# Kernel tuning notes

Hardware: AMD Instinct MI355X
Metric: run time of the kernel (lower is better)

The kernel has to match this reference:

```python
import jax, jax.numpy as jnp
import numpy as np

INPUT_SIZE = 512   # num_embeddings == RNN input feature dim
SEQ = INPUT_SIZE // 4   # 128, embedding dim == RNN seq_len
HID = 12
OUT = 3
B = 2048


def setup_inputs() -> dict:
    key = jax.random.key(0)
    ks = jax.random.split(key, 12)
    s = 0.1
    x = jax.random.randint(ks[0], (B, INPUT_SIZE), 0, INPUT_SIZE)
    emb = jax.random.normal(ks[1], (INPUT_SIZE, SEQ), dtype=jnp.float32) * s
    w_ih_f = jax.random.normal(ks[2], (HID, INPUT_SIZE), dtype=jnp.float32) * s
    w_hh_f = jax.random.normal(ks[3], (HID, HID), dtype=jnp.float32) * s
    b_ih_f = jax.random.normal(ks[4], (HID,), dtype=jnp.float32) * s
    b_hh_f = jax.random.normal(ks[5], (HID,), dtype=jnp.float32) * s
    w_ih_r = jax.random.normal(ks[6], (HID, INPUT_SIZE), dtype=jnp.float32) * s
    w_hh_r = jax.random.normal(ks[7], (HID, HID), dtype=jnp.float32) * s
    b_ih_r = jax.random.normal(ks[8], (HID,), dtype=jnp.float32) * s
    b_hh_r = jax.random.normal(ks[9], (HID,), dtype=jnp.float32) * s
    fc_w = jax.random.normal(ks[10], (OUT, 2 * HID), dtype=jnp.float32) * s
    fc_b = jax.random.normal(ks[11], (OUT,), dtype=jnp.float32) * s
    return {"x": x, "emb": emb,
            "w_ih_f": w_ih_f, "w_hh_f": w_hh_f, "b_ih_f": b_ih_f, "b_hh_f": b_hh_f,
            "w_ih_r": w_ih_r, "w_hh_r": w_hh_r, "b_ih_r": b_ih_r, "b_hh_r": b_hh_r,
            "fc_w": fc_w, "fc_b": fc_b}


def reference(x, emb, w_ih_f, w_hh_f, b_ih_f, b_hh_f,
              w_ih_r, w_hh_r, b_ih_r, b_hh_r, fc_w, fc_b):
    # embedding lookup: (B, INPUT_SIZE) -> (B, INPUT_SIZE, SEQ)
    e = emb[x]
    # view(-1, input_size, seq) is a no-op on this contiguous shape; swapaxes(1,2)
    xs = jnp.swapaxes(e, 1, 2)  # (B, SEQ, INPUT_SIZE): seq_len=SEQ, feat=INPUT_SIZE

    # forward-direction tanh RNN: precompute input projections, scan the recurrence
    pre = jnp.einsum('bsi,hi->sbh', xs, w_ih_f) + b_ih_f  # (SEQ, B, HID)

    def step(h, p):
        h = jnp.tanh(p + h @ w_hh_f.T + b_hh_f)
        return h, None

    h0 = jnp.zeros((xs.shape[0], HID), dtype=xs.dtype)
    h_fwd, _ = jax.lax.scan(step, h0, pre)  # final forward hidden (B, HID)

    # reverse-direction output at the LAST timestep = one step from zero hidden
    # on x_{T-1} (only out[:, -1, :] is consumed by the module)
    h_bwd = jnp.tanh(xs[:, -1, :] @ w_ih_r.T + b_ih_r + b_hh_r)  # (B, HID)

    out_last = jnp.concatenate([h_fwd, h_bwd], axis=-1)  # (B, 2*HID)
    return out_last @ fc_w.T + fc_b  # (B, OUT)
```

## Files before the change

kernel.cpp:

```cpp
#include <hip/hip_runtime.h>
#include <hip/hip_bf16.h>

#define B_N     2048
#define IN_N    512
#define SEQ_N   128
#define HID_N   12
#define HP_N    16
#define OUT_N   3

typedef __attribute__((ext_vector_type(8))) short short8;
typedef __attribute__((ext_vector_type(4))) float f32x4;
typedef unsigned int uint;
typedef unsigned short ushort;

__device__ __forceinline__ float fast_tanh(float x) {
    float e = __builtin_amdgcn_exp2f(x * 2.8853900817779268f);
    return 1.0f - 2.0f * __builtin_amdgcn_rcpf(e + 1.0f);
}

__device__ __forceinline__ ushort f2bf(float f) {
    uint u = __float_as_uint(f);
    u += 0x7fffu + ((u >> 16) & 1u);
    return (ushort)(u >> 16);
}

__device__ __forceinline__ float bf2f(ushort s) {
    return __uint_as_float(((uint)s) << 16);
}

__global__ __launch_bounds__(256) void k_prep(
    const float* __restrict__ emb, const float* __restrict__ w_ih_f,
    const float* __restrict__ w_ih_r,
    ushort* __restrict__ embB, ushort* __restrict__ wBT, ushort* __restrict__ wRT)
{
    int tid = blockIdx.x * 256 + threadIdx.x;
    float4 e = ((const float4*)emb)[tid];
    uint2 o;
    o.x = (uint)f2bf(e.x) | ((uint)f2bf(e.y) << 16);
    o.y = (uint)f2bf(e.z) | ((uint)f2bf(e.w) << 16);
    ((uint2*)embB)[tid] = o;
    if (tid < 16 * IN_N) {
        bool live = tid < HID_N * IN_N;
        wBT[tid] = live ? f2bf(w_ih_f[tid]) : (ushort)0;
        wRT[tid] = live ? f2bf(w_ih_r[tid]) : (ushort)0;
    }
}

__global__ __launch_bounds__(256, 2) void k_pre(
    const int* __restrict__ x, const ushort* __restrict__ embB,
    const ushort* __restrict__ wBT, const ushort* __restrict__ wRT,
    const float* __restrict__ b_ih_r, const float* __restrict__ b_hh_r,
    ushort* __restrict__ preB, float* __restrict__ rev)
{
    __shared__ int xb[IN_N];
    __shared__ __align__(16) ushort As[128 * 128];

    const int t = threadIdx.x;
    const int b = blockIdx.x;

    ((int2*)xb)[t] = ((const int2*)(x + b * IN_N))[t];
    __syncthreads();

    const int l      = t & 63;
    const int w      = t >> 6;
    const int lane16 = l & 15;
    const int quad   = l >> 4;
    const int il     = w * 32 + quad * 8;
    const int wg     = w * 4 + quad;
    const int wsx    = lane16 & 7;

    f32x4 acc[2] = {{0.f,0.f,0.f,0.f},{0.f,0.f,0.f,0.f}};
    f32x4 accR   = {0.f,0.f,0.f,0.f};

    uint R[8][4];

    #pragma unroll
    for (int j = 0; j < 8; ++j) {
        const uint4 v = *(const uint4*)(embB + (size_t)xb[il + j] * SEQ_N + lane16 * 8);
        R[j][0] = v.x; R[j][1] = v.y; R[j][2] = v.z; R[j][3] = v.w;
    }

    for (int c = 0; c < 4; ++c) {
        short8 bfr[4], bfrR[4];
        #pragma unroll
        for (int ks = 0; ks < 4; ++ks) {
            bfr[ks]  = *(const short8*)(wBT + lane16 * IN_N + c * 128 + ks * 32 + quad * 8);
            bfrR[ks] = *(const short8*)(wRT + lane16 * IN_N + c * 128 + ks * 32 + quad * 8);
        }

        if (c) __syncthreads();

        #pragma unroll
        for (int p = 0; p < 8; ++p) {
            const uint sel = (p & 1) ? 0x07060302u : 0x05040100u;
            const int pv = p >> 1;
            uint u0 = __builtin_amdgcn_perm(R[1][pv], R[0][pv], sel);
            uint u1 = __builtin_amdgcn_perm(R[3][pv], R[2][pv], sel);
            uint u2 = __builtin_amdgcn_perm(R[5][pv], R[4][pv], sel);
            uint u3 = __builtin_amdgcn_perm(R[7][pv], R[6][pv], sel);
            const int s = lane16 * 8 + p;
            *(uint4*)&As[(size_t)s * 128 + (size_t)(wg ^ wsx) * 8] =
                make_uint4(u0, u1, u2, u3);
        }

        if (c < 3) {
            const int ibase = (c + 1) * 128 + il;
            #pragma unroll
            for (int j = 0; j < 8; ++j) {
                const uint4 v = *(const uint4*)(embB + (size_t)xb[ibase + j] * SEQ_N + lane16 * 8);
                R[j][0] = v.x; R[j][1] = v.y; R[j][2] = v.z; R[j][3] = v.w;
            }
        }
        __syncthreads();

        #pragma unroll
        for (int tt = 0; tt < 2; ++tt) {
            const int row = (w * 2 + tt) * 16 + lane16;
            const int rsx = (row >> 3) & 7;
            #pragma unroll
            for (int ks = 0; ks < 4; ++ks) {
                short8 af = *(const short8*)&As[(size_t)row * 128 +
                                                (size_t)(((ks * 4 + quad) ^ rsx)) * 8];
                acc[tt] = __builtin_amdgcn_mfma_f32_16x16x32_bf16(af, bfr[ks], acc[tt], 0, 0, 0);
                if (tt == 1)
                    accR = __builtin_amdgcn_mfma_f32_16x16x32_bf16(af, bfrR[ks], accR, 0, 0, 0);
            }
        }
    }

    if (lane16 < HID_N) {
        #pragma unroll
        for (int tt = 0; tt < 2; ++tt) {
            #pragma unroll
            for (int r = 0; r < 4; ++r) {
                int s = (w * 2 + tt) * 16 + quad * 4 + r;
                preB[((size_t)b * SEQ_N + s) * HP_N + lane16] = f2bf(acc[tt][r]);
            }
        }
        if (w == 3 && quad == 3)
            rev[b * HP_N + lane16] =
                fast_tanh(accR[3] + b_ih_r[lane16] + b_hh_r[lane16]);
    }
}

__global__ __launch_bounds__(256) void k_rnn(
    const ushort* __restrict__ preB, const float* __restrict__ rev,
    const float* __restrict__ w_hh_f,
    const float* __restrict__ b_ih_f, const float* __restrict__ b_hh_f,
    const float* __restrict__ fc_w, const float* __restrict__ fc_b,
    float* __restrict__ out)
{
    __shared__ float ho[16][40];

    const int tid = threadIdx.x;
    const int l   = tid & 63;
    const int j   = l & 15;
    const int jj  = (j < 12) ? j : 0;
    const int gid = tid >> 4;
    const int b   = blockIdx.x * 16 + gid;
    const int baseaddr = (l & 48) << 2;

    const float4* wr = (const float4*)(w_hh_f + jj * 12);
    float4 w0 = wr[0], w1 = wr[1], w2 = wr[2];
    float W[12] = {w0.x, w0.y, w0.z, w0.w, w1.x, w1.y, w1.z, w1.w,
                   w2.x, w2.y, w2.z, w2.w};
    const float bias = b_ih_f[jj] + b_hh_f[jj];

    const ushort* pb = preB + (size_t)b * SEQ_N * HP_N + j;
    ushort pq[8];
    #pragma unroll
    for (int k = 0; k < 8; ++k) pq[k] = pb[k * HP_N];

    float h = 0.f;
    for (int s8 = 0; s8 < 16; ++s8) {
        #pragma unroll
        for (int k = 0; k < 8; ++k) {
            int s = s8 * 8 + k;
            float p = bf2f(pq[k]) + bias;
            pq[k] = pb[((s + 8) & 127) * HP_N];
            int hb = __float_as_int(h);
            float hk[12];
            #pragma unroll
            for (int kk = 0; kk < 12; ++kk)
                hk[kk] = __int_as_float(__builtin_amdgcn_ds_bpermute(baseaddr + 4 * kk, hb));
            float c0 = p, c1 = 0.f, c2 = 0.f;
            #pragma unroll
            for (int u = 0; u < 4; ++u) {
                c0 = __builtin_fmaf(W[u],     hk[u],     c0);
                c1 = __builtin_fmaf(W[4 + u], hk[4 + u], c1);
                c2 = __builtin_fmaf(W[8 + u], hk[8 + u], c2);
            }
            h = fast_tanh(c0 + c1 + c2);
        }
    }

    ho[gid][j]      = h;
    ho[gid][20 + j] = rev[b * HP_N + j];
    if (j < OUT_N) {
        const float* fw = fc_w + j * 24;
        float o = fc_b[j];
        #pragma unroll
        for (int k = 0; k < 12; ++k)
            o += fw[k] * ho[gid][k] + fw[12 + k] * ho[gid][20 + k];
        out[b * OUT_N + j] = o;
    }
}

extern "C" void kernel_launch(void* const* d_in, const int* in_sizes, int n_in,
                              void* d_out, int out_size, void* d_ws, size_t ws_size,
                              hipStream_t stream) {
    const int*   x      = (const int*)  d_in[0];
    const float* emb    = (const float*)d_in[1];
    const float* w_ih_f = (const float*)d_in[2];
    const float* w_hh_f = (const float*)d_in[3];
    const float* b_ih_f = (const float*)d_in[4];
    const float* b_hh_f = (const float*)d_in[5];
    const float* w_ih_r = (const float*)d_in[6];
    const float* b_ih_r = (const float*)d_in[8];
    const float* b_hh_r = (const float*)d_in[9];
    const float* fc_w   = (const float*)d_in[10];
    const float* fc_b   = (const float*)d_in[11];
    float* out = (float*)d_out;

    ushort* preB = (ushort*)d_ws;
    float*  rev  = (float*)((char*)d_ws + 8388608);
    ushort* embB = (ushort*)((char*)d_ws + 8519680);
    ushort* wBT  = (ushort*)((char*)d_ws + 8650752);
    ushort* wRT  = (ushort*)((char*)d_ws + 8667136);

    k_prep<<<64,   256, 0, stream>>>(emb, w_ih_f, w_ih_r, embB, wBT, wRT);
    k_pre <<<B_N,  256, 0, stream>>>(x, embB, wBT, wRT, b_ih_r, b_hh_r, preB, rev);
    k_rnn <<<B_N/16,256,0, stream>>>(preB, rev, w_hh_f, b_ih_f, b_hh_f, fc_w, fc_b, out);
}
```

Measured before the change: 138.2 us.

## Prepack MFMA weight fragments, fix LDS swizzle conflicts, raise k_pre occupancy

The ih weights are now prepacked into per-lane MFMA B-fragment order, so each lane reads one contiguous 16-byte chunk per k-step instead of strided rows. The LDS swizzle for the A tile now also XORs in the row's low bits, to spread the ds_write/ds_read traffic across banks. launch_bounds for k_pre goes from 2 to 4 blocks per SM to allow more occupancy, at the risk of register pressure or spills with the R[8][4] staging array.

```diff
diff --git a/kernel.cpp b/kernel.cpp
--- a/kernel.cpp
+++ b/kernel.cpp
@@ -31,7 +31,7 @@
 __global__ __launch_bounds__(256) void k_prep(
     const float* __restrict__ emb, const float* __restrict__ w_ih_f,
     const float* __restrict__ w_ih_r,
-    ushort* __restrict__ embB, ushort* __restrict__ wBT, ushort* __restrict__ wRT)
+    ushort* __restrict__ embB, ushort* __restrict__ wP)
 {
     int tid = blockIdx.x * 256 + threadIdx.x;
     float4 e = ((const float4*)emb)[tid];
@@ -39,16 +39,21 @@
     o.x = (uint)f2bf(e.x) | ((uint)f2bf(e.y) << 16);
     o.y = (uint)f2bf(e.z) | ((uint)f2bf(e.w) << 16);
     ((uint2*)embB)[tid] = o;
-    if (tid < 16 * IN_N) {
-        bool live = tid < HID_N * IN_N;
-        wBT[tid] = live ? f2bf(w_ih_f[tid]) : (ushort)0;
-        wRT[tid] = live ? f2bf(w_ih_r[tid]) : (ushort)0;
-    }
-}
-
-__global__ __launch_bounds__(256, 2) void k_pre(
+
+    int j   = tid & 7;
+    int l   = (tid >> 3) & 63;
+    int src = (tid >> 9) & 1;
+    int cks = tid >> 10;
+    int h   = l & 15;
+    int i   = (cks >> 2) * 128 + (cks & 3) * 32 + (l >> 4) * 8 + j;
+    const float* wsrc = src ? w_ih_r : w_ih_f;
+    wP[(((size_t)cks * 2 + src) * 64 + l) * 8 + j] =
+        (h < HID_N) ? f2bf(wsrc[h * IN_N + i]) : (ushort)0;
+}
+
+__global__ __launch_bounds__(256, 4) void k_pre(
     const int* __restrict__ x, const ushort* __restrict__ embB,
-    const ushort* __restrict__ wBT, const ushort* __restrict__ wRT,
+    const ushort* __restrict__ wP,
     const float* __restrict__ b_ih_r, const float* __restrict__ b_hh_r,
     ushort* __restrict__ preB, float* __restrict__ rev)
 {
@@ -67,7 +72,7 @@
     const int quad   = l >> 4;
     const int il     = w * 32 + quad * 8;
     const int wg     = w * 4 + quad;
-    const int wsx    = lane16 & 7;
+    const int l7     = lane16 & 7;
 
     f32x4 acc[2] = {{0.f,0.f,0.f,0.f},{0.f,0.f,0.f,0.f}};
     f32x4 accR   = {0.f,0.f,0.f,0.f};
@@ -84,8 +89,9 @@
         short8 bfr[4], bfrR[4];
         #pragma unroll
         for (int ks = 0; ks < 4; ++ks) {
-            bfr[ks]  = *(const short8*)(wBT + lane16 * IN_N + c * 128 + ks * 32 + quad * 8);
-            bfrR[ks] = *(const short8*)(wRT + lane16 * IN_N + c * 128 + ks * 32 + quad * 8);
+            const ushort* wp = wP + ((size_t)(c * 4 + ks) * 128 + l) * 8;
+            bfr[ks]  = *(const short8*)(wp);
+            bfrR[ks] = *(const short8*)(wp + 512);
         }
 
         if (c) __syncthreads();
@@ -98,8 +104,9 @@
             uint u1 = __builtin_amdgcn_perm(R[3][pv], R[2][pv], sel);
             uint u2 = __builtin_amdgcn_perm(R[5][pv], R[4][pv], sel);
             uint u3 = __builtin_amdgcn_perm(R[7][pv], R[6][pv], sel);
-            const int s = lane16 * 8 + p;
-            *(uint4*)&As[(size_t)s * 128 + (size_t)(wg ^ wsx) * 8] =
+            const int s    = lane16 * 8 + p;
+            const int slot = wg ^ p ^ l7;
+            *(uint4*)&As[(size_t)s * 128 + (size_t)slot * 8] =
                 make_uint4(u0, u1, u2, u3);
         }
 
@@ -116,11 +123,11 @@
         #pragma unroll
         for (int tt = 0; tt < 2; ++tt) {
             const int row = (w * 2 + tt) * 16 + lane16;
-            const int rsx = (row >> 3) & 7;
+            const int fr  = (row & 7) ^ ((row >> 3) & 7);
             #pragma unroll
             for (int ks = 0; ks < 4; ++ks) {
-                short8 af = *(const short8*)&As[(size_t)row * 128 +
-                                                (size_t)(((ks * 4 + quad) ^ rsx)) * 8];
+                const int slot = (ks * 4 + quad) ^ fr;
+                short8 af = *(const short8*)&As[(size_t)row * 128 + (size_t)slot * 8];
                 acc[tt] = __builtin_amdgcn_mfma_f32_16x16x32_bf16(af, bfr[ks], acc[tt], 0, 0, 0);
                 if (tt == 1)
                     accR = __builtin_amdgcn_mfma_f32_16x16x32_bf16(af, bfrR[ks], accR, 0, 0, 0);
@@ -225,10 +232,9 @@
     ushort* preB = (ushort*)d_ws;
     float*  rev  = (float*)((char*)d_ws + 8388608);
     ushort* embB = (ushort*)((char*)d_ws + 8519680);
-    ushort* wBT  = (ushort*)((char*)d_ws + 8650752);
-    ushort* wRT  = (ushort*)((char*)d_ws + 8667136);
-
-    k_prep<<<64,   256, 0, stream>>>(emb, w_ih_f, w_ih_r, embB, wBT, wRT);
-    k_pre <<<B_N,  256, 0, stream>>>(x, embB, wBT, wRT, b_ih_r, b_hh_r, preB, rev);
+    ushort* wP   = (ushort*)((char*)d_ws + 8650752);
+
+    k_prep<<<64,   256, 0, stream>>>(emb, w_ih_f, w_ih_r, embB, wP);
+    k_pre <<<B_N,  256, 0, stream>>>(x, embB, wP, b_ih_r, b_hh_r, preB, rev);
     k_rnn <<<B_N/16,256,0, stream>>>(preB, rev, w_hh_f, b_ih_f, b_hh_f, fc_w, fc_b, out);
 }
```

Result: faster. 127.1 us (-8.0%).
